# Optimization experiments

Hardware: AMD Instinct MI355X
Metric: run time of the kernel (lower is better)

## Reference

```python
import jax, jax.numpy as jnp
from jax import lax
import numpy as np

N_BATCH = 1024
FEATURE_NUM = 128
NUM_CLASSES = 1000
MAX_MODES = 10
TEMPERATURE = 1.0
NU = FEATURE_NUM // 2 - 1  # p/2 - 1 = 63


def log_ive_pair(x):
    """Vectorized Miller downward recurrence, done in log domain for stability
    (equivalent to the torch code's dynamic rescaling-by-log trick).
    Returns (log Ive_NU(x), log Ive_{NU+1}(x)) elementwise over x."""
    logx = jnp.log(x)
    z = jnp.zeros_like(x)
    init = (z, jnp.full_like(x, -jnp.inf), z, z)  # logI_{2nu}=0, logI_{2nu+1}=-inf
    i_vals = jnp.arange(2 * NU, 0, -1)

    def step(carry, i):
        logI, logI1, s0, s1 = carry
        fi = i.astype(logx.dtype)
        # I_{i-1} = (2 i / x) I_i + I_{i+1}  ->  logaddexp in log domain
        new_logI = jnp.logaddexp(jnp.log(2.0 * fi) - logx + logI, logI1)
        # after the update, old logI is log I_i; record at i==NU and i==NU+1
        s0 = jnp.where(i == NU, logI, s0)
        s1 = jnp.where(i == NU + 1, logI, s1)
        return (new_logI, logI, s0, s1), None

    (logI0, _, s0, s1), _ = lax.scan(step, init, i_vals)
    log_ive0 = jnp.log(jax.scipy.special.i0e(x))
    return log_ive0 + s0 - logI0, log_ive0 + s1 - logI0


@jax.custom_vjp
def log_ratio_c(k, logc):
    lognu, _ = log_ive_pair(k)
    return lognu + k - NU * jnp.log(k + 1e-20) - logc


def _lrc_fwd(k, logc):
    lognu, lognu1 = log_ive_pair(k)
    out = lognu + k - NU * jnp.log(k + 1e-20) - logc
    # custom backward of LogRatioC: grad wrt k = min(I_{nu+1}/I_nu, 1); None wrt logc
    return out, (jnp.minimum(jnp.exp(lognu1 - lognu), 1.0), jnp.zeros_like(logc))


def _lrc_bwd(res, g):
    ratio, zlogc = res
    return (ratio * g, zlogc)


log_ratio_c.defvjp(_lrc_fwd, _lrc_bwd)


def _forward(features, Ave_old, Amount_old, labels):
    # --- soft_assign_mode on detached features vs. old prototypes ---
    f_d = lax.stop_gradient(features)
    ave_sel = Ave_old[labels]  # [N, M, D] gather by label
    num = jnp.einsum('nd,nmd->nm', f_d, ave_sel)
    den = jnp.maximum(jnp.linalg.norm(f_d, axis=1, keepdims=True)
                      * jnp.linalg.norm(ave_sel, axis=2), 1e-8)
    soft = jax.nn.softmax(num / den / TEMPERATURE, axis=1)  # [N, M]
    # --- update_CV (estimator_old): label-indexed scatter of soft assignments ---
    sum_oh = jax.ops.segment_sum(soft, labels, num_segments=NUM_CLASSES)  # [C, M]
    wfeat = jax.ops.segment_sum(soft[:, :, None] * f_d[:, None, :], labels,
                                num_segments=NUM_CLASSES)  # [C, M, D]
    ave_cma = wfeat / jnp.where(sum_oh == 0, 1.0, sum_oh)[:, :, None]
    w = sum_oh / (sum_oh + Amount_old)
    w = jnp.where(jnp.isnan(w), 0.0, w)
    Ave = lax.stop_gradient(Ave_old * (1.0 - w[:, :, None]) + ave_cma * w[:, :, None])
    # --- update_kappa: vMF concentration + Bessel recurrence for log normalizer ---
    R = jnp.linalg.norm(Ave, axis=2)  # [C, M]
    kappa = FEATURE_NUM * R / (1.0 - R * R)
    kappa = jnp.where((kappa > 1e5) | (kappa < 0), 1e5, kappa)
    lognu, _ = log_ive_pair(kappa)
    logc = lognu + kappa - NU * jnp.log(kappa + 1e-20)
    # --- contrastive logits ---
    Ave_n = Ave / jnp.maximum(jnp.linalg.norm(Ave, axis=2, keepdims=True), 1e-12)
    sims = features @ Ave_n.reshape(NUM_CLASSES * MAX_MODES, FEATURE_NUM).T / TEMPERATURE
    kf = kappa.reshape(-1)  # [C*M]
    kappa_new = jnp.sqrt(kf * kf + 2.0 * kf * sims + 1.0)  # [N, C*M]
    logits = log_ratio_c(kappa_new, logc.reshape(-1))
    return jnp.max(logits.reshape(-1, NUM_CLASSES, MAX_MODES), axis=2)  # [N, C]


def setup_inputs() -> dict:
    key = jax.random.key(0)
    k1, k2, k3 = jax.random.split(key, 3)
    features = jax.random.normal(k1, (N_BATCH, FEATURE_NUM), dtype=jnp.float32)
    features = features / jnp.linalg.norm(features, axis=1, keepdims=True)
    Ave_old = jax.random.normal(k2, (NUM_CLASSES, MAX_MODES, FEATURE_NUM), dtype=jnp.float32)
    Ave_old = 0.9 * Ave_old / jnp.linalg.norm(Ave_old, axis=2, keepdims=True)  # R<1 so kappa>0
    Amount_old = 100.0 * jnp.ones((NUM_CLASSES, MAX_MODES), dtype=jnp.float32)
    labels = jax.random.randint(k3, (N_BATCH,), 0, NUM_CLASSES, dtype=jnp.int32)
    return {"features": features, "Ave_old": Ave_old, "Amount_old": Amount_old, "labels": labels}


def reference(features, Ave_old, Amount_old, labels):
    return _forward(features, Ave_old, Amount_old, labels)
```

## Files before the change

kernel.cpp:

```cpp
#include <hip/hip_runtime.h>
#include <math.h>

#define C_NUM 1000
#define M_MODES 10
#define CMTOT (C_NUM * M_MODES)
#define D_FEAT 128
#define N_BATCH 1024

typedef _Float16 h16;
typedef h16 h16x2 __attribute__((ext_vector_type(2)));
typedef h16 half8 __attribute__((ext_vector_type(8)));
typedef float f32x4 __attribute__((ext_vector_type(4)));

#define OFF_FEATH  0
#define OFF_AVEH   65536
#define OFF_CMC    705536

__global__ __launch_bounds__(256) void prep(
    const float* __restrict__ feat,
    const float* __restrict__ ave_old,
    const float* __restrict__ amount,
    const int*   __restrict__ labels,
    h16*   __restrict__ feat_h,
    h16*   __restrict__ ave_h,
    float* __restrict__ cmc)
{
    const int wave = threadIdx.x >> 6;
    const int lane = threadIdx.x & 63;
    const float2* feat2 = (const float2*)feat;
    const float2* ave2  = (const float2*)ave_old;

    if (blockIdx.x >= 250) {
        const int n = (blockIdx.x - 250) * 4 + wave;
        float2 f = feat2[n * 64 + lane];
        ((h16x2*)(feat_h + n * D_FEAT))[lane] = (h16x2){(h16)f.x, (h16)f.y};
        return;
    }

    const int c = blockIdx.x * 4 + wave;

    float2 ao[M_MODES];
    #pragma unroll
    for (int t = 0; t < M_MODES; ++t) ao[t] = ave2[(c * M_MODES + t) * 64 + lane];

    float an[M_MODES];
    #pragma unroll
    for (int t = 0; t < M_MODES; ++t) an[t] = ao[t].x * ao[t].x + ao[t].y * ao[t].y;
    #pragma unroll
    for (int s = 1; s < 64; s <<= 1)
        #pragma unroll
        for (int t = 0; t < M_MODES; ++t) an[t] += __shfl_xor(an[t], s);
    #pragma unroll
    for (int t = 0; t < M_MODES; ++t) an[t] = sqrtf(an[t]);

    float ssum[M_MODES], wx[M_MODES], wy[M_MODES];
    #pragma unroll
    for (int t = 0; t < M_MODES; ++t) { ssum[t] = 0.f; wx[t] = 0.f; wy[t] = 0.f; }

    const int4* lab4 = (const int4*)labels;
    #pragma unroll
    for (int k4 = 0; k4 < 4; ++k4) {
        int4 lv = lab4[lane + k4 * 64];
        #pragma unroll
        for (int j = 0; j < 4; ++j) {
            int lbl = (j == 0) ? lv.x : (j == 1) ? lv.y : (j == 2) ? lv.z : lv.w;
            unsigned long long mask = __ballot(lbl == c);
            while (mask) {
                int lz = __ffsll((long long)mask) - 1;
                mask &= mask - 1;
                const int n = 4 * lz + 256 * k4 + j;
                float2 f = feat2[n * 64 + lane];
                float d[M_MODES], fn = f.x * f.x + f.y * f.y;
                #pragma unroll
                for (int t = 0; t < M_MODES; ++t)
                    d[t] = f.x * ao[t].x + f.y * ao[t].y;
                #pragma unroll
                for (int s = 1; s < 64; s <<= 1) {
                    fn += __shfl_xor(fn, s);
                    #pragma unroll
                    for (int t = 0; t < M_MODES; ++t) d[t] += __shfl_xor(d[t], s);
                }
                const float fnorm = sqrtf(fn);
                float sc[M_MODES], mx = -INFINITY;
                #pragma unroll
                for (int t = 0; t < M_MODES; ++t) {
                    float den = fmaxf(fnorm * an[t], 1e-8f);
                    sc[t] = d[t] / den;
                    mx = fmaxf(mx, sc[t]);
                }
                float se = 0.f;
                #pragma unroll
                for (int t = 0; t < M_MODES; ++t) { sc[t] = __expf(sc[t] - mx); se += sc[t]; }
                const float inv = 1.0f / se;
                #pragma unroll
                for (int t = 0; t < M_MODES; ++t) {
                    float sm = sc[t] * inv;
                    ssum[t] += sm;
                    wx[t] = fmaf(sm, f.x, wx[t]);
                    wy[t] = fmaf(sm, f.y, wy[t]);
                }
            }
        }
    }

    float r2[M_MODES];
    #pragma unroll
    for (int t = 0; t < M_MODES; ++t) {
        const float am = amount[c * M_MODES + t];
        float w = ssum[t] / (ssum[t] + am);
        if (!(w == w)) w = 0.0f;
        const float dn = (ssum[t] == 0.0f) ? 1.0f : ssum[t];
        float ax = ao[t].x * (1.0f - w) + (wx[t] / dn) * w;
        float ay = ao[t].y * (1.0f - w) + (wy[t] / dn) * w;
        ao[t].x = ax; ao[t].y = ay;
        r2[t] = ax * ax + ay * ay;
    }
    #pragma unroll
    for (int s = 1; s < 64; s <<= 1)
        #pragma unroll
        for (int t = 0; t < M_MODES; ++t) r2[t] += __shfl_xor(r2[t], s);

    #pragma unroll
    for (int t = 0; t < M_MODES; ++t) {
        const float R   = sqrtf(r2[t]);
        const float nrm = fmaxf(R, 1e-12f);
        ((h16x2*)(ave_h + (c * M_MODES + t) * D_FEAT))[lane] =
            (h16x2){(h16)(ao[t].x / nrm), (h16)(ao[t].y / nrm)};
    }

    if (lane < M_MODES) {
        float myr2 = 0.f;
        #pragma unroll
        for (int t = 0; t < M_MODES; ++t) if (lane == t) myr2 = r2[t];
        const float R = sqrtf(myr2);
        float kappa = 128.0f * R / (1.0f - R * R);
        if (kappa > 1e5f || kappa < 0.0f) kappa = 1e5f;
        float k   = kappa;
        float swk = sqrtf(fmaf(k, k, 3969.0f));
        float i1  = 1.0f / (63.0f + swk);
        float i2  = 1.0f / swk;
        float c1  = 1.0f - 63.0f * i1 - 0.5f * i2;
        float c2  = 31.5f * i1 * i1 + 0.25f * i2 * i2;
        float c3  = -(21.0f * i1 * i1 * i1 + (1.0f / 6.0f) * i2 * i2 * i2);
        float4* p = (float4*)(cmc + (c * M_MODES + lane) * 8);
        p[0] = make_float4(2.0f * k, fmaf(k, k, 3970.0f), swk, c1);
        p[1] = make_float4(c2, c3, 0.0f, 0.0f);
    }
}

#define SWZ(row, j) (((row) << 8) + ((((j) ^ ((row) & 15))) << 4))
#define LSTR 81
__global__ __launch_bounds__(512) void k3_logits(
    const h16*   __restrict__ feat_h,
    const h16*   __restrict__ ave_h,
    const float* __restrict__ cmc,
    float* __restrict__ out)
{
    __shared__ __align__(16) char smem[128 * 256 + 80 * 256];
    char*  smemB = smem + 128 * 256;
    float* ls    = (float*)smem;

    const int tid    = threadIdx.x;
    const int cmbase = blockIdx.x * 80;
    const int nbase  = blockIdx.y * 128;

    {
        const float4* src = (const float4*)(feat_h + nbase * D_FEAT);
        #pragma unroll
        for (int i = 0; i < 4; ++i) {
            int e = tid + i * 512;
            int r = e >> 4, j = e & 15;
            *(float4*)(smem + SWZ(r, j)) = src[e];
        }
    }
    for (int e = tid; e < 1280; e += 512) {
        int r = e >> 4, j = e & 15;
        *(float4*)(smemB + SWZ(r, j)) = ((const float4*)(ave_h + cmbase * D_FEAT))[e];
    }
    __syncthreads();

    const int wave = tid >> 6;
    const int lane = tid & 63;
    const int lrow = lane & 15;
    const int lhi  = lane >> 4;

    f32x4 acc[5] = {};
    #pragma unroll
    for (int ks = 0; ks < 4; ++ks) {
        half8 a = *(const half8*)(smem + SWZ(wave * 16 + lrow, ks * 4 + lhi));
        #pragma unroll
        for (int t = 0; t < 5; ++t) {
            half8 b = *(const half8*)(smemB + SWZ(t * 16 + lrow, ks * 4 + lhi));
            acc[t] = __builtin_amdgcn_mfma_f32_16x16x32_f16(a, b, acc[t], 0, 0, 0);
        }
    }

    #pragma unroll
    for (int t = 0; t < 5; ++t) {
        const int cm = cmbase + t * 16 + lrow;
        float4 p0 = ((const float4*)(cmc + cm * 8))[0];
        float4 p1 = ((const float4*)(cmc + cm * 8))[1];
        #pragma unroll
        for (int r = 0; r < 4; ++r) {
            float s   = acc[t][r];
            float swn = sqrtf(fmaf(p0.x, s, p0.y));
            float num = fmaf(p0.x, s, 1.0f);
            float D   = __fdividef(num, swn + p0.z);
            acc[t][r] = D * fmaf(D, fmaf(D, p1.y, p1.x), p0.w);
        }
    }

    __syncthreads();
    #pragma unroll
    for (int t = 0; t < 5; ++t)
        #pragma unroll
        for (int r = 0; r < 4; ++r)
            ls[(wave * 16 + lhi * 4 + r) * LSTR + t * 16 + lrow] = acc[t][r];
    __syncthreads();

    #pragma unroll
    for (int rep = 0; rep < 2; ++rep) {
        int id = rep * 512 + tid;
        int q  = id >> 3;
        int cl = id & 7;
        const float* row = ls + q * LSTR + cl * 10;
        float mx = row[0];
        #pragma unroll
        for (int j = 1; j < 10; ++j) mx = fmaxf(mx, row[j]);
        out[(nbase + q) * C_NUM + blockIdx.x * 8 + cl] = mx;
    }
}

extern "C" void kernel_launch(void* const* d_in, const int* in_sizes, int n_in,
                              void* d_out, int out_size, void* d_ws, size_t ws_size,
                              hipStream_t stream) {
    const float* feat    = (const float*)d_in[0];
    const float* ave_old = (const float*)d_in[1];
    const float* amount  = (const float*)d_in[2];
    const int*   labels  = (const int*)d_in[3];
    float* out = (float*)d_out;
    float* ws  = (float*)d_ws;

    h16*   feat_h = (h16*)(ws + OFF_FEATH);
    h16*   ave_h  = (h16*)(ws + OFF_AVEH);
    float* cmc    = ws + OFF_CMC;

    prep<<<dim3(506), dim3(256), 0, stream>>>(
        feat, ave_old, amount, labels, feat_h, ave_h, cmc);

    k3_logits<<<dim3(125, 8), dim3(512), 0, stream>>>(
        feat_h, ave_h, cmc, out);
}
```

Before: 100.6 us.

## Fuse prototype update into logits kernel and keep per-mode constants in shared memory

Moves the per-class prototype update, normalization and kappa constant computation into the logits kernel, writing the half-precision prototypes and constants directly into shared memory instead of global workspace. Feature conversion becomes its own small kernel. This removes the global write/read of prototypes and constants and lets load of features overlap with prototype math, at the cost of recomputing each class's update once per batch row-block (8x redundancy).

```diff
diff --git a/kernel.cpp b/kernel.cpp
--- a/kernel.cpp
+++ b/kernel.cpp
@@ -3,7 +3,6 @@
 
 #define C_NUM 1000
 #define M_MODES 10
-#define CMTOT (C_NUM * M_MODES)
 #define D_FEAT 128
 #define N_BATCH 1024
 
@@ -13,35 +12,50 @@
 typedef float f32x4 __attribute__((ext_vector_type(4)));
 
 #define OFF_FEATH  0
-#define OFF_AVEH   65536
-#define OFF_CMC    705536
-
-__global__ __launch_bounds__(256) void prep(
+
+__global__ __launch_bounds__(256) void feat_cvt(
+    const float* __restrict__ feat, h16* __restrict__ feat_h)
+{
+    const int n    = blockIdx.x * 4 + (threadIdx.x >> 6);
+    const int lane = threadIdx.x & 63;
+    float2 f = ((const float2*)feat)[n * 64 + lane];
+    ((h16x2*)(feat_h + n * D_FEAT))[lane] = (h16x2){(h16)f.x, (h16)f.y};
+}
+
+#define SWZ(row, j) (((row) << 8) + ((((j) ^ ((row) & 15))) << 4))
+#define LSTR 81
+__global__ __launch_bounds__(512, 4) void k3_fused(
+    const h16*   __restrict__ feat_h,
     const float* __restrict__ feat,
     const float* __restrict__ ave_old,
     const float* __restrict__ amount,
     const int*   __restrict__ labels,
-    h16*   __restrict__ feat_h,
-    h16*   __restrict__ ave_h,
-    float* __restrict__ cmc)
+    float* __restrict__ out)
 {
-    const int wave = threadIdx.x >> 6;
-    const int lane = threadIdx.x & 63;
+    __shared__ __align__(16) char smem[128 * 256 + 80 * 256 + 6 * 80 * 4];
+    char*  smemB = smem + 128 * 256;
+    float* cmcs  = (float*)(smem + 128 * 256 + 80 * 256);
+    float* ls    = (float*)smem;
+
+    const int tid    = threadIdx.x;
+    const int wave   = tid >> 6;
+    const int lane   = tid & 63;
+    const int cmbase = blockIdx.x * 80;
+    const int nbase  = blockIdx.y * 128;
+    const int cls    = blockIdx.x * 8 + wave;
+
     const float2* feat2 = (const float2*)feat;
     const float2* ave2  = (const float2*)ave_old;
 
-    if (blockIdx.x >= 250) {
-        const int n = (blockIdx.x - 250) * 4 + wave;
-        float2 f = feat2[n * 64 + lane];
-        ((h16x2*)(feat_h + n * D_FEAT))[lane] = (h16x2){(h16)f.x, (h16)f.y};
-        return;
-    }
-
-    const int c = blockIdx.x * 4 + wave;
-
     float2 ao[M_MODES];
     #pragma unroll
-    for (int t = 0; t < M_MODES; ++t) ao[t] = ave2[(c * M_MODES + t) * 64 + lane];
+    for (int t = 0; t < M_MODES; ++t) ao[t] = ave2[(cls * M_MODES + t) * 64 + lane];
+
+    float4 av0, av1, av2_, av3;
+    {
+        const float4* src = (const float4*)(feat_h + nbase * D_FEAT);
+        av0 = src[tid]; av1 = src[tid + 512]; av2_ = src[tid + 1024]; av3 = src[tid + 1536];
+    }
 
     float an[M_MODES];
     #pragma unroll
@@ -53,18 +67,26 @@
     #pragma unroll
     for (int t = 0; t < M_MODES; ++t) an[t] = sqrtf(an[t]);
 
+    {
+        int e, r, j;
+        e = tid;        r = e >> 4; j = e & 15; *(float4*)(smem + SWZ(r, j)) = av0;
+        e = tid + 512;  r = e >> 4; j = e & 15; *(float4*)(smem + SWZ(r, j)) = av1;
+        e = tid + 1024; r = e >> 4; j = e & 15; *(float4*)(smem + SWZ(r, j)) = av2_;
+        e = tid + 1536; r = e >> 4; j = e & 15; *(float4*)(smem + SWZ(r, j)) = av3;
+    }
+
     float ssum[M_MODES], wx[M_MODES], wy[M_MODES];
     #pragma unroll
     for (int t = 0; t < M_MODES; ++t) { ssum[t] = 0.f; wx[t] = 0.f; wy[t] = 0.f; }
 
     const int4* lab4 = (const int4*)labels;
-    #pragma unroll
+    #pragma unroll 1
     for (int k4 = 0; k4 < 4; ++k4) {
         int4 lv = lab4[lane + k4 * 64];
         #pragma unroll
         for (int j = 0; j < 4; ++j) {
             int lbl = (j == 0) ? lv.x : (j == 1) ? lv.y : (j == 2) ? lv.z : lv.w;
-            unsigned long long mask = __ballot(lbl == c);
+            unsigned long long mask = __ballot(lbl == cls);
             while (mask) {
                 int lz = __ffsll((long long)mask) - 1;
                 mask &= mask - 1;
@@ -106,7 +128,7 @@
     float r2[M_MODES];
     #pragma unroll
     for (int t = 0; t < M_MODES; ++t) {
-        const float am = amount[c * M_MODES + t];
+        const float am = amount[cls * M_MODES + t];
         float w = ssum[t] / (ssum[t] + am);
         if (!(w == w)) w = 0.0f;
         const float dn = (ssum[t] == 0.0f) ? 1.0f : ssum[t];
@@ -124,8 +146,9 @@
     for (int t = 0; t < M_MODES; ++t) {
         const float R   = sqrtf(r2[t]);
         const float nrm = fmaxf(R, 1e-12f);
-        ((h16x2*)(ave_h + (c * M_MODES + t) * D_FEAT))[lane] =
-            (h16x2){(h16)(ao[t].x / nrm), (h16)(ao[t].y / nrm)};
+        const int   r   = wave * M_MODES + t;
+        char* dst = smemB + SWZ(r, lane >> 2) + ((lane * 4) & 15);
+        *(h16x2*)dst = (h16x2){(h16)(ao[t].x / nrm), (h16)(ao[t].y / nrm)};
     }
 
     if (lane < M_MODES) {
@@ -139,48 +162,16 @@
         float swk = sqrtf(fmaf(k, k, 3969.0f));
         float i1  = 1.0f / (63.0f + swk);
         float i2  = 1.0f / swk;
-        float c1  = 1.0f - 63.0f * i1 - 0.5f * i2;
-        float c2  = 31.5f * i1 * i1 + 0.25f * i2 * i2;
-        float c3  = -(21.0f * i1 * i1 * i1 + (1.0f / 6.0f) * i2 * i2 * i2);
-        float4* p = (float4*)(cmc + (c * M_MODES + lane) * 8);
-        p[0] = make_float4(2.0f * k, fmaf(k, k, 3970.0f), swk, c1);
-        p[1] = make_float4(c2, c3, 0.0f, 0.0f);
-    }
-}
-
-#define SWZ(row, j) (((row) << 8) + ((((j) ^ ((row) & 15))) << 4))
-#define LSTR 81
-__global__ __launch_bounds__(512) void k3_logits(
-    const h16*   __restrict__ feat_h,
-    const h16*   __restrict__ ave_h,
-    const float* __restrict__ cmc,
-    float* __restrict__ out)
-{
-    __shared__ __align__(16) char smem[128 * 256 + 80 * 256];
-    char*  smemB = smem + 128 * 256;
-    float* ls    = (float*)smem;
-
-    const int tid    = threadIdx.x;
-    const int cmbase = blockIdx.x * 80;
-    const int nbase  = blockIdx.y * 128;
-
-    {
-        const float4* src = (const float4*)(feat_h + nbase * D_FEAT);
-        #pragma unroll
-        for (int i = 0; i < 4; ++i) {
-            int e = tid + i * 512;
-            int r = e >> 4, j = e & 15;
-            *(float4*)(smem + SWZ(r, j)) = src[e];
-        }
-    }
-    for (int e = tid; e < 1280; e += 512) {
-        int r = e >> 4, j = e & 15;
-        *(float4*)(smemB + SWZ(r, j)) = ((const float4*)(ave_h + cmbase * D_FEAT))[e];
+        const int cmL = wave * M_MODES + lane;
+        cmcs[0 * 80 + cmL] = 2.0f * k;
+        cmcs[1 * 80 + cmL] = fmaf(k, k, 3970.0f);
+        cmcs[2 * 80 + cmL] = swk;
+        cmcs[3 * 80 + cmL] = 1.0f - 63.0f * i1 - 0.5f * i2;
+        cmcs[4 * 80 + cmL] = 31.5f * i1 * i1 + 0.25f * i2 * i2;
+        cmcs[5 * 80 + cmL] = -(21.0f * i1 * i1 * i1 + (1.0f / 6.0f) * i2 * i2 * i2);
     }
     __syncthreads();
 
-    const int wave = tid >> 6;
-    const int lane = tid & 63;
     const int lrow = lane & 15;
     const int lhi  = lane >> 4;
 
@@ -197,16 +188,20 @@
 
     #pragma unroll
     for (int t = 0; t < 5; ++t) {
-        const int cm = cmbase + t * 16 + lrow;
-        float4 p0 = ((const float4*)(cmc + cm * 8))[0];
-        float4 p1 = ((const float4*)(cmc + cm * 8))[1];
+        const int cmL = t * 16 + lrow;
+        const float c2k = cmcs[0 * 80 + cmL];
+        const float k2p = cmcs[1 * 80 + cmL];
+        const float swk = cmcs[2 * 80 + cmL];
+        const float c1  = cmcs[3 * 80 + cmL];
+        const float c2  = cmcs[4 * 80 + cmL];
+        const float c3  = cmcs[5 * 80 + cmL];
         #pragma unroll
         for (int r = 0; r < 4; ++r) {
             float s   = acc[t][r];
-            float swn = sqrtf(fmaf(p0.x, s, p0.y));
-            float num = fmaf(p0.x, s, 1.0f);
-            float D   = __fdividef(num, swn + p0.z);
-            acc[t][r] = D * fmaf(D, fmaf(D, p1.y, p1.x), p0.w);
+            float swn = sqrtf(fmaf(c2k, s, k2p));
+            float num = fmaf(c2k, s, 1.0f);
+            float D   = __fdividef(num, swn + swk);
+            acc[t][r] = D * fmaf(D, fmaf(D, c3, c2), c1);
         }
     }
 
@@ -241,13 +236,10 @@
     float* out = (float*)d_out;
     float* ws  = (float*)d_ws;
 
-    h16*   feat_h = (h16*)(ws + OFF_FEATH);
-    h16*   ave_h  = (h16*)(ws + OFF_AVEH);
-    float* cmc    = ws + OFF_CMC;
-
-    prep<<<dim3(506), dim3(256), 0, stream>>>(
-        feat, ave_old, amount, labels, feat_h, ave_h, cmc);
-
-    k3_logits<<<dim3(125, 8), dim3(512), 0, stream>>>(
-        feat_h, ave_h, cmc, out);
+    h16* feat_h = (h16*)(ws + OFF_FEATH);
+
+    feat_cvt<<<dim3(256), dim3(256), 0, stream>>>(feat, feat_h);
+
+    k3_fused<<<dim3(125, 8), dim3(512), 0, stream>>>(
+        feat_h, feat, ave_old, amount, labels, out);
 }
```

After: 122.3 us. 1.22x slower.
